# Optimization experiments

Measured on AMD Instinct MI355X. Metric: run time of the kernel, lower is better.

## Reference

```python
import jax, jax.numpy as jnp
import numpy as np

B, F, N = 16, 64, 32768
C0, C1, C2 = 64, 16, 1
TOP_K = 64
EPS = 1e-5


def setup_inputs() -> dict:
    key = jax.random.key(0)
    ks = jax.random.split(key, 6)
    def rn(k, shape, scale=1.0):
        return jax.random.normal(k, shape, dtype=jnp.float32) * scale
    return {
        "sortvec": rn(ks[0], (B, 1, F, N)),
        "input": rn(ks[1], (B, F, N)),
        # conv0: kernel (F,1), in=1, out=64 -> weight reduces to [C0, F]
        "w0": rn(ks[2], (C0, F), np.sqrt(2.0 / F)), "b0": jnp.zeros((C0,), jnp.float32),
        "w1": rn(ks[3], (C1, C0), np.sqrt(2.0 / C0)), "b1": jnp.zeros((C1,), jnp.float32),
        "w2": rn(ks[4], (C2, C1), np.sqrt(2.0 / C1)), "b2": jnp.zeros((C2,), jnp.float32),
        "g0": jnp.ones((C0,), jnp.float32), "bt0": jnp.zeros((C0,), jnp.float32),
        "g1": jnp.ones((C1,), jnp.float32), "bt1": jnp.zeros((C1,), jnp.float32),
        "g2": jnp.ones((C2,), jnp.float32), "bt2": jnp.zeros((C2,), jnp.float32),
    }


def _bn_relu(x, g, b):
    # training-mode BatchNorm2d over (B, N) per channel; x: [B, C, N]
    mu = jnp.mean(x, axis=(0, 2), keepdims=True)
    var = jnp.var(x, axis=(0, 2), keepdims=True)
    return jax.nn.relu((x - mu) * jax.lax.rsqrt(var + EPS) * g[None, :, None] + b[None, :, None])


def reference(sortvec, input, w0, b0, w1, b1, w2, b2, g0, bt0, g1, bt1, g2, bt2):
    # conv0 with kernel (F,1) collapses the feature axis: [B,1,F,N] -> [B,C0,N]
    x = jnp.einsum('bfn,of->bon', sortvec[:, 0], w0) + b0[None, :, None]
    x = _bn_relu(x, g0, bt0)
    x = _bn_relu(jnp.einsum('bcn,oc->bon', x, w1) + b1[None, :, None], g1, bt1)
    score = _bn_relu(jnp.einsum('bcn,oc->bon', x, w2) + b2[None, :, None], g2, bt2)  # [B,1,N]
    _, idx = jax.lax.top_k(score[:, 0], TOP_K)                                        # [B,K]
    sorted_input = jnp.take_along_axis(input, idx[:, None, :], axis=2)                # [B,F,K]
    sorted_score = jnp.take_along_axis(score, idx[:, None, :], axis=2)                # [B,1,K]
    feat = jnp.concatenate([sorted_input, sorted_score], axis=1)                      # [B,F+1,K]
    return feat, idx
```

## Files before the change

kernel.cpp:

```cpp
#include <hip/hip_runtime.h>


constexpr int   B_   = 16;
constexpr int   F_   = 64;
constexpr int   N_   = 32768;
constexpr int   C0_  = 64;
constexpr int   C1_  = 16;
constexpr int   K_   = 64;
constexpr long long S_ = (long long)B_ * N_;
constexpr float EPS_ = 1e-5f;

constexpr int NB0 = 1024;
constexpr int NB1 = 2048;
constexpr int NB2 = 2048;
constexpr int T64 = 8192;

__global__ __launch_bounds__(256) void k_prep(const float* __restrict__ w0,
                                              const float* __restrict__ w1,
                                              float* __restrict__ w0T,
                                              float* __restrict__ w1T) {
  int t = threadIdx.x;
  for (int e = t; e < 64 * 64; e += 256) {
    int o = e >> 6, f = e & 63;
    w0T[f * 64 + o] = w0[e];
  }
  for (int e = t; e < 16 * 64; e += 256) {
    int o = e >> 6, c = e & 63;
    w1T[c * 16 + o] = w1[e];
  }
}

__global__ __launch_bounds__(256) void k_stat0(const float* __restrict__ sv,
                                               const float* __restrict__ w0T,
                                               const float* __restrict__ b0,
                                               float* __restrict__ p0) {
  __shared__ float svt[64][64];
  const int t  = threadIdx.x;
  const int p  = t & 63;
  const int cg = __builtin_amdgcn_readfirstlane(t >> 6);

  float bb[16];
#pragma unroll
  for (int j = 0; j < 16; ++j) bb[j] = b0[cg * 16 + j];

  float s1[16], s2[16];
#pragma unroll
  for (int j = 0; j < 16; ++j) { s1[j] = 0.f; s2[j] = 0.f; }

  for (int tile = blockIdx.x; tile < T64; tile += NB0) {
    const int b  = tile >> 9;
    const int n0 = (tile & 511) << 6;
    const float* src = sv + ((long long)b * 64) * N_ + n0;
    __syncthreads();
#pragma unroll
    for (int q = 0; q < 4; ++q) {
      int e = t + q * 256;
      int f = e >> 4, c4 = (e & 15) << 2;
      *(float4*)&svt[f][c4] = *(const float4*)(src + (long long)f * N_ + c4);
    }
    __syncthreads();

    float y[16];
#pragma unroll
    for (int j = 0; j < 16; ++j) y[j] = bb[j];
    for (int f = 0; f < 64; ++f) {
      float s = svt[f][p];
      const float* wr = w0T + f * 64 + cg * 16;
#pragma unroll
      for (int j = 0; j < 16; ++j) y[j] = fmaf(wr[j], s, y[j]);
    }
#pragma unroll
    for (int j = 0; j < 16; ++j) {
      s1[j] += y[j];
      s2[j] = fmaf(y[j], y[j], s2[j]);
    }
  }

#pragma unroll
  for (int j = 0; j < 16; ++j) {
#pragma unroll
    for (int off = 32; off; off >>= 1) {
      s1[j] += __shfl_down(s1[j], off, 64);
      s2[j] += __shfl_down(s2[j], off, 64);
    }
  }
  if (p == 0) {
    float* dst = p0 + (long long)blockIdx.x * 128;
#pragma unroll
    for (int j = 0; j < 16; ++j) {
      dst[cg * 16 + j]      = s1[j];
      dst[64 + cg * 16 + j] = s2[j];
    }
  }
}

__global__ __launch_bounds__(128) void k_reduce0(const float* __restrict__ p0,
                                                 const float* __restrict__ g,
                                                 const float* __restrict__ bt,
                                                 float* __restrict__ st) {
  __shared__ float l[128];
  int j = threadIdx.x;
  float a0 = 0.f, a1 = 0.f, a2 = 0.f, a3 = 0.f;
  for (int i = 0; i < NB0; i += 4) {
    a0 += p0[(long long)(i + 0) * 128 + j];
    a1 += p0[(long long)(i + 1) * 128 + j];
    a2 += p0[(long long)(i + 2) * 128 + j];
    a3 += p0[(long long)(i + 3) * 128 + j];
  }
  l[j] = (a0 + a1) + (a2 + a3);
  __syncthreads();
  if (j < 64) {
    const float inv = 1.f / (float)S_;
    float mean = l[j] * inv;
    float ex2  = l[64 + j] * inv;
    float var  = ex2 - mean * mean;
    float sc   = g[j] * rsqrtf(var + EPS_);
    st[j]      = sc;
    st[64 + j] = bt[j] - mean * sc;
  }
}

__global__ __launch_bounds__(256) void k_layer01(const float* __restrict__ sv,
                                                 const float* __restrict__ w0T,
                                                 const float* __restrict__ b0,
                                                 const float* __restrict__ st0,
                                                 const float* __restrict__ w1T,
                                                 const float* __restrict__ b1,
                                                 float* __restrict__ y1,
                                                 float* __restrict__ p1) {
  __shared__ float svt[64][64];
  __shared__ float h0[64][64];
  const int t  = threadIdx.x;
  const int p  = t & 63;
  const int cg = __builtin_amdgcn_readfirstlane(t >> 6);

  float bb[16], sc[16], sh[16];
#pragma unroll
  for (int j = 0; j < 16; ++j) {
    bb[j] = b0[cg * 16 + j];
    sc[j] = st0[cg * 16 + j];
    sh[j] = st0[64 + cg * 16 + j];
  }
  float bb1[4];
#pragma unroll
  for (int j = 0; j < 4; ++j) bb1[j] = b1[cg * 4 + j];

  float s1[4], s2[4];
#pragma unroll
  for (int j = 0; j < 4; ++j) { s1[j] = 0.f; s2[j] = 0.f; }

  for (int tile = blockIdx.x; tile < T64; tile += NB1) {
    const int b  = tile >> 9;
    const int n0 = (tile & 511) << 6;
    const float* src = sv + ((long long)b * 64) * N_ + n0;
    __syncthreads();
#pragma unroll
    for (int q = 0; q < 4; ++q) {
      int e = t + q * 256;
      int f = e >> 4, c4 = (e & 15) << 2;
      *(float4*)&svt[f][c4] = *(const float4*)(src + (long long)f * N_ + c4);
    }
    __syncthreads();

    float y[16];
#pragma unroll
    for (int j = 0; j < 16; ++j) y[j] = bb[j];
    for (int f = 0; f < 64; ++f) {
      float s = svt[f][p];
      const float* wr = w0T + f * 64 + cg * 16;
#pragma unroll
      for (int j = 0; j < 16; ++j) y[j] = fmaf(wr[j], s, y[j]);
    }
#pragma unroll
    for (int j = 0; j < 16; ++j) {
      float h = fmaf(y[j], sc[j], sh[j]);
      h0[cg * 16 + j][p] = h > 0.f ? h : 0.f;
    }
    __syncthreads();

    float z[4];
#pragma unroll
    for (int j = 0; j < 4; ++j) z[j] = bb1[j];
    for (int f = 0; f < 64; ++f) {
      float h = h0[f][p];
      const float* wr = w1T + f * 16 + cg * 4;
#pragma unroll
      for (int j = 0; j < 4; ++j) z[j] = fmaf(wr[j], h, z[j]);
    }
#pragma unroll
    for (int j = 0; j < 4; ++j) {
      s1[j] += z[j];
      s2[j] = fmaf(z[j], z[j], s2[j]);
      y1[((long long)b * 16 + cg * 4 + j) * N_ + n0 + p] = z[j];
    }
  }

#pragma unroll
  for (int j = 0; j < 4; ++j) {
#pragma unroll
    for (int off = 32; off; off >>= 1) {
      s1[j] += __shfl_down(s1[j], off, 64);
      s2[j] += __shfl_down(s2[j], off, 64);
    }
  }
  if (p == 0) {
    float* dst = p1 + (long long)blockIdx.x * 32;
#pragma unroll
    for (int j = 0; j < 4; ++j) {
      dst[cg * 4 + j]      = s1[j];
      dst[16 + cg * 4 + j] = s2[j];
    }
  }
}

__global__ __launch_bounds__(64) void k_reduce1(const float* __restrict__ p1,
                                                const float* __restrict__ g,
                                                const float* __restrict__ bt,
                                                float* __restrict__ st) {
  __shared__ float l[32];
  int j = threadIdx.x;
  if (j < 32) {
    float a0 = 0.f, a1 = 0.f, a2 = 0.f, a3 = 0.f;
    for (int i = 0; i < NB1; i += 4) {
      a0 += p1[(long long)(i + 0) * 32 + j];
      a1 += p1[(long long)(i + 1) * 32 + j];
      a2 += p1[(long long)(i + 2) * 32 + j];
      a3 += p1[(long long)(i + 3) * 32 + j];
    }
    l[j] = (a0 + a1) + (a2 + a3);
  }
  __syncthreads();
  if (j < 16) {
    const float inv = 1.f / (float)S_;
    float mean = l[j] * inv;
    float ex2  = l[16 + j] * inv;
    float var  = ex2 - mean * mean;
    float sc   = g[j] * rsqrtf(var + EPS_);
    st[j]      = sc;
    st[16 + j] = bt[j] - mean * sc;
  }
}

__global__ __launch_bounds__(256) void k_layer2(const float* __restrict__ y1,
                                                const float* __restrict__ st1,
                                                const float* __restrict__ w2,
                                                const float* __restrict__ b2,
                                                float* __restrict__ y2,
                                                float* __restrict__ p2) {
  __shared__ float yt[16][256];
  __shared__ float ls[4], lq[4];
  const int t    = threadIdx.x;
  const int tile = blockIdx.x;
  const int b    = tile >> 7;
  const int n0   = (tile & 127) << 8;
  const float* src = y1 + ((long long)b * 16) * N_ + n0;
#pragma unroll
  for (int q = 0; q < 4; ++q) {
    int e = t + q * 256;
    int c = e >> 6, c4 = (e & 63) << 2;
    *(float4*)&yt[c][c4] = *(const float4*)(src + (long long)c * N_ + c4);
  }
  __syncthreads();

  float acc = b2[0];
#pragma unroll
  for (int c = 0; c < 16; ++c) {
    float h = fmaf(yt[c][t], st1[c], st1[16 + c]);
    h = h > 0.f ? h : 0.f;
    acc = fmaf(w2[c], h, acc);
  }
  y2[(long long)b * N_ + n0 + t] = acc;

  float ss = acc, sq = acc * acc;
#pragma unroll
  for (int off = 32; off; off >>= 1) {
    ss += __shfl_down(ss, off, 64);
    sq += __shfl_down(sq, off, 64);
  }
  int wid = t >> 6, lid = t & 63;
  if (lid == 0) { ls[wid] = ss; lq[wid] = sq; }
  __syncthreads();
  if (t == 0) {
    p2[(long long)blockIdx.x * 2 + 0] = (ls[0] + ls[1]) + (ls[2] + ls[3]);
    p2[(long long)blockIdx.x * 2 + 1] = (lq[0] + lq[1]) + (lq[2] + lq[3]);
  }
}

__global__ __launch_bounds__(1024) void k_topk(const float* __restrict__ y2,
                                               const float* __restrict__ p2,
                                               const float* __restrict__ g2,
                                               const float* __restrict__ bt2,
                                               const float* __restrict__ inp,
                                               float* __restrict__ out) {
  __shared__ float rr[1024];
  __shared__ unsigned long long wbest[16];
  __shared__ int   idxs[K_];
  __shared__ float scores[K_];
  __shared__ float s2s[2];

  const int t = threadIdx.x;
  const int b = blockIdx.x;

  {
    int comp = t >> 9;
    int j    = t & 511;
    float a = p2[(long long)(j)        * 2 + comp] +
              p2[(long long)(j + 512)  * 2 + comp] +
              p2[(long long)(j + 1024) * 2 + comp] +
              p2[(long long)(j + 1536) * 2 + comp];
    rr[t] = a;
    __syncthreads();
    for (int s = 256; s > 0; s >>= 1) {
      if (j < s) rr[t] = rr[t] + rr[t + s];
      __syncthreads();
    }
    if (t == 0) {
      const float inv = 1.f / (float)S_;
      float mean = rr[0] * inv;
      float ex2  = rr[512] * inv;
      float var  = ex2 - mean * mean;
      float scv  = g2[0] * rsqrtf(var + EPS_);
      s2s[0] = scv;
      s2s[1] = bt2[0] - mean * scv;
    }
    __syncthreads();
  }
  const float scale2 = s2s[0], shift2 = s2s[1];

  const float* yrow = y2 + (long long)b * N_;
  unsigned long long key[32];
  unsigned long long cur = 0ull;
#pragma unroll
  for (int i = 0; i < 32; ++i) {
    int idx = (i << 10) | t;
    float v = yrow[idx];
    unsigned u = __float_as_uint(v);
    u = (u & 0x80000000u) ? ~u : (u | 0x80000000u);
    unsigned long long k = ((unsigned long long)u << 32) | (unsigned)(N_ - 1 - idx);
    key[i] = k;
    cur = k > cur ? k : cur;
  }

  const int wid = t >> 6, lid = t & 63;
  for (int r = 0; r < K_; ++r) {
    unsigned long long m = cur;
#pragma unroll
    for (int off = 32; off; off >>= 1) {
      unsigned long long o = __shfl_xor(m, off, 64);
      m = o > m ? o : m;
    }
    if (lid == 0) wbest[wid] = m;
    __syncthreads();
    unsigned long long w = wbest[0];
#pragma unroll
    for (int i = 1; i < 16; ++i) {
      unsigned long long x = wbest[i];
      w = x > w ? x : w;
    }
    const int idx = N_ - 1 - (int)(w & 0xffffffffu);
    if (t == 0) {
      idxs[r] = idx;
      unsigned u = (unsigned)(w >> 32);
      u = (u & 0x80000000u) ? (u & 0x7fffffffu) : ~u;
      float v = __uint_as_float(u);
      float s = fmaf(v, scale2, shift2);
      scores[r] = s > 0.f ? s : 0.f;
    }
    if ((idx & 1023) == t) {
      const int slot = idx >> 10;
#pragma unroll
      for (int i2 = 0; i2 < 32; ++i2)
        if (i2 == slot) key[i2] = 0ull;
      unsigned long long c2 = 0ull;
#pragma unroll
      for (int i2 = 0; i2 < 32; ++i2) c2 = key[i2] > c2 ? key[i2] : c2;
      cur = c2;
    }
    __syncthreads();
  }

  const float* ib = inp + ((long long)b * 64) * N_;
  for (int e = t; e < 65 * 64; e += 1024) {
    int f = e >> 6, k = e & 63;
    float val = (f < 64) ? ib[(long long)f * N_ + idxs[k]] : scores[k];
    out[((long long)b * 65 + f) * 64 + k] = val;
  }
  if (t < K_) out[(long long)B_ * 65 * 64 + b * 64 + t] = (float)idxs[t];
}

extern "C" void kernel_launch(void* const* d_in, const int* in_sizes, int n_in,
                              void* d_out, int out_size, void* d_ws, size_t ws_size,
                              hipStream_t stream) {
  const float* sv  = (const float*)d_in[0];
  const float* inp = (const float*)d_in[1];
  const float* w0  = (const float*)d_in[2];
  const float* b0  = (const float*)d_in[3];
  const float* w1  = (const float*)d_in[4];
  const float* b1  = (const float*)d_in[5];
  const float* w2  = (const float*)d_in[6];
  const float* b2  = (const float*)d_in[7];
  const float* g0  = (const float*)d_in[8];
  const float* bt0 = (const float*)d_in[9];
  const float* g1  = (const float*)d_in[10];
  const float* bt1 = (const float*)d_in[11];
  const float* g2  = (const float*)d_in[12];
  const float* bt2 = (const float*)d_in[13];
  float* out = (float*)d_out;

  float* ws  = (float*)d_ws;
  float* y1  = ws;
  float* y2  = y1 + (size_t)S_ * 16;
  float* p0  = y2 + (size_t)S_;
  float* p1  = p0 + (size_t)NB0 * 128;
  float* p2  = p1 + (size_t)NB1 * 32;
  float* st0 = p2 + (size_t)NB2 * 2;
  float* st1 = st0 + 128;
  float* w0T = st1 + 32;
  float* w1T = w0T + 4096;

  k_prep   <<<1,    256, 0, stream>>>(w0, w1, w0T, w1T);
  k_stat0  <<<NB0,  256, 0, stream>>>(sv, w0T, b0, p0);
  k_reduce0<<<1,    128, 0, stream>>>(p0, g0, bt0, st0);
  k_layer01<<<NB1,  256, 0, stream>>>(sv, w0T, b0, st0, w1T, b1, y1, p1);
  k_reduce1<<<1,     64, 0, stream>>>(p1, g1, bt1, st1);
  k_layer2 <<<NB2,  256, 0, stream>>>(y1, st1, w2, b2, y2, p2);
  k_topk   <<<B_,  1024, 0, stream>>>(y2, p2, g2, bt2, inp, out);
}
```

Baseline: 332.2 us.

## Replace iterative block top-k with histogram threshold, candidate compaction and wave-level select

The score kernel now also builds a per-batch 4096-bin histogram of order-preserving score keys in shared memory and merges it into a global histogram. A threshold kernel then finds the bin that holds the 64th-largest score. A compaction kernel appends only the scores at or above that bin to a small per-batch candidate buffer, and a single wave selects the top 64 from those candidates. This replaces 64 block-wide argmax rounds over 32768 elements, each with barriers and only 16 blocks running. The trade-off is three extra launches, a memset, global atomics, and a fixed candidate capacity of 1024 that would silently drop entries if the threshold bin is too crowded.

```diff
diff --git a/kernel.cpp b/kernel.cpp
--- a/kernel.cpp
+++ b/kernel.cpp
@@ -2,18 +2,22 @@
 
 
 constexpr int   B_   = 16;
-constexpr int   F_   = 64;
 constexpr int   N_   = 32768;
-constexpr int   C0_  = 64;
-constexpr int   C1_  = 16;
 constexpr int   K_   = 64;
 constexpr long long S_ = (long long)B_ * N_;
 constexpr float EPS_ = 1e-5f;
 
-constexpr int NB0 = 1024;
-constexpr int NB1 = 2048;
-constexpr int NB2 = 2048;
-constexpr int T64 = 8192;
+constexpr int NB0   = 1024;
+constexpr int NB1   = 2048;
+constexpr int NB2   = 128;
+constexpr int T64   = 8192;
+constexpr int NBINS = 4096;
+constexpr int CAP   = 1024;
+
+__device__ __forceinline__ unsigned key_map(float f) {
+  unsigned u = __float_as_uint(f);
+  return (u & 0x80000000u) ? ~u : (u | 0x80000000u);
+}
 
 __global__ __launch_bounds__(256) void k_prep(const float* __restrict__ w0,
                                               const float* __restrict__ w1,
@@ -241,107 +245,169 @@
   }
 }
 
-__global__ __launch_bounds__(256) void k_layer2(const float* __restrict__ y1,
-                                                const float* __restrict__ st1,
-                                                const float* __restrict__ w2,
-                                                const float* __restrict__ b2,
-                                                float* __restrict__ y2,
-                                                float* __restrict__ p2) {
-  __shared__ float yt[16][256];
-  __shared__ float ls[4], lq[4];
-  const int t    = threadIdx.x;
-  const int tile = blockIdx.x;
-  const int b    = tile >> 7;
-  const int n0   = (tile & 127) << 8;
-  const float* src = y1 + ((long long)b * 16) * N_ + n0;
-#pragma unroll
-  for (int q = 0; q < 4; ++q) {
-    int e = t + q * 256;
-    int c = e >> 6, c4 = (e & 63) << 2;
-    *(float4*)&yt[c][c4] = *(const float4*)(src + (long long)c * N_ + c4);
-  }
+__global__ __launch_bounds__(1024) void k_layer2(const float* __restrict__ y1,
+                                                 const float* __restrict__ st1,
+                                                 const float* __restrict__ w2,
+                                                 const float* __restrict__ b2,
+                                                 float* __restrict__ y2,
+                                                 float* __restrict__ p2,
+                                                 int* __restrict__ ghist) {
+  __shared__ int hist[NBINS];
+  __shared__ float ls[16], lq[16];
+  const int t   = threadIdx.x;
+  const int blk = blockIdx.x;
+  const int b   = blk >> 3;
+  const int n0  = ((blk & 7) << 12) | (t << 2);
+
+#pragma unroll
+  for (int i = 0; i < NBINS / 1024; ++i) hist[t + i * 1024] = 0;
+
+  float sc[16], sh[16], w[16];
+#pragma unroll
+  for (int c = 0; c < 16; ++c) { sc[c] = st1[c]; sh[c] = st1[16 + c]; w[c] = w2[c]; }
+  const float bias = b2[0];
+
+  float a0 = bias, a1 = bias, a2 = bias, a3 = bias;
+  const float* base = y1 + ((long long)b * 16) * N_ + n0;
+#pragma unroll
+  for (int c = 0; c < 16; ++c) {
+    float4 v = *(const float4*)(base + (long long)c * N_);
+    float h;
+    h = fmaf(v.x, sc[c], sh[c]); h = h > 0.f ? h : 0.f; a0 = fmaf(w[c], h, a0);
+    h = fmaf(v.y, sc[c], sh[c]); h = h > 0.f ? h : 0.f; a1 = fmaf(w[c], h, a1);
+    h = fmaf(v.z, sc[c], sh[c]); h = h > 0.f ? h : 0.f; a2 = fmaf(w[c], h, a2);
+    h = fmaf(v.w, sc[c], sh[c]); h = h > 0.f ? h : 0.f; a3 = fmaf(w[c], h, a3);
+  }
+  float4 o; o.x = a0; o.y = a1; o.z = a2; o.w = a3;
+  *(float4*)(y2 + (long long)b * N_ + n0) = o;
+
   __syncthreads();
 
-  float acc = b2[0];
-#pragma unroll
-  for (int c = 0; c < 16; ++c) {
-    float h = fmaf(yt[c][t], st1[c], st1[16 + c]);
-    h = h > 0.f ? h : 0.f;
-    acc = fmaf(w2[c], h, acc);
-  }
-  y2[(long long)b * N_ + n0 + t] = acc;
-
-  float ss = acc, sq = acc * acc;
+  atomicAdd(&hist[key_map(a0) >> 20], 1);
+  atomicAdd(&hist[key_map(a1) >> 20], 1);
+  atomicAdd(&hist[key_map(a2) >> 20], 1);
+  atomicAdd(&hist[key_map(a3) >> 20], 1);
+
+  float ss = (a0 + a1) + (a2 + a3);
+  float sq = fmaf(a0, a0, fmaf(a1, a1, fmaf(a2, a2, a3 * a3)));
 #pragma unroll
   for (int off = 32; off; off >>= 1) {
     ss += __shfl_down(ss, off, 64);
     sq += __shfl_down(sq, off, 64);
   }
-  int wid = t >> 6, lid = t & 63;
+  const int wid = t >> 6, lid = t & 63;
   if (lid == 0) { ls[wid] = ss; lq[wid] = sq; }
   __syncthreads();
   if (t == 0) {
-    p2[(long long)blockIdx.x * 2 + 0] = (ls[0] + ls[1]) + (ls[2] + ls[3]);
-    p2[(long long)blockIdx.x * 2 + 1] = (lq[0] + lq[1]) + (lq[2] + lq[3]);
-  }
-}
-
-__global__ __launch_bounds__(1024) void k_topk(const float* __restrict__ y2,
-                                               const float* __restrict__ p2,
-                                               const float* __restrict__ g2,
-                                               const float* __restrict__ bt2,
-                                               const float* __restrict__ inp,
-                                               float* __restrict__ out) {
-  __shared__ float rr[1024];
-  __shared__ unsigned long long wbest[16];
-  __shared__ int   idxs[K_];
-  __shared__ float scores[K_];
-  __shared__ float s2s[2];
-
-  const int t = threadIdx.x;
-  const int b = blockIdx.x;
-
-  {
-    int comp = t >> 9;
-    int j    = t & 511;
-    float a = p2[(long long)(j)        * 2 + comp] +
-              p2[(long long)(j + 512)  * 2 + comp] +
-              p2[(long long)(j + 1024) * 2 + comp] +
-              p2[(long long)(j + 1536) * 2 + comp];
-    rr[t] = a;
-    __syncthreads();
-    for (int s = 256; s > 0; s >>= 1) {
-      if (j < s) rr[t] = rr[t] + rr[t + s];
-      __syncthreads();
-    }
-    if (t == 0) {
-      const float inv = 1.f / (float)S_;
-      float mean = rr[0] * inv;
-      float ex2  = rr[512] * inv;
-      float var  = ex2 - mean * mean;
-      float scv  = g2[0] * rsqrtf(var + EPS_);
-      s2s[0] = scv;
-      s2s[1] = bt2[0] - mean * scv;
-    }
-    __syncthreads();
-  }
-  const float scale2 = s2s[0], shift2 = s2s[1];
-
-  const float* yrow = y2 + (long long)b * N_;
-  unsigned long long key[32];
+    float Sv = 0.f, Qv = 0.f;
+#pragma unroll
+    for (int i = 0; i < 16; ++i) { Sv += ls[i]; Qv += lq[i]; }
+    p2[blk * 2 + 0] = Sv;
+    p2[blk * 2 + 1] = Qv;
+  }
+#pragma unroll
+  for (int i = 0; i < NBINS / 1024; ++i) {
+    int v = hist[t + i * 1024];
+    if (v) atomicAdd(&ghist[b * NBINS + t + i * 1024], v);
+  }
+}
+
+__global__ __launch_bounds__(256) void k_thresh(const int* __restrict__ ghist,
+                                                int* __restrict__ Tb) {
+  __shared__ int hl[NBINS + NBINS / 64];
+  const int t = threadIdx.x, b = blockIdx.x;
+  const int* h = ghist + b * NBINS;
+  for (int i = t; i < NBINS; i += 256) hl[i + (i >> 6)] = h[i];
+  __syncthreads();
+  if (t < 64) {
+    const int l = t;
+    int s = 0;
+    for (int j = 0; j < 64; ++j) s += hl[(l * 64 + j) + l];
+    int Sv = s;
+#pragma unroll
+    for (int off = 1; off < 64; off <<= 1) {
+      int v = __shfl_down(Sv, off, 64);
+      if (l + off < 64) Sv += v;
+    }
+    unsigned long long m = __ballot(Sv >= K_);
+    const int lstar = 63 - __builtin_clzll(m);
+    const int tailS = (lstar < 63) ? __shfl(Sv, lstar + 1, 64) : 0;
+    int Tj = hl[(lstar * 64 + l) + lstar];
+#pragma unroll
+    for (int off = 1; off < 64; off <<= 1) {
+      int v = __shfl_down(Tj, off, 64);
+      if (l + off < 64) Tj += v;
+    }
+    const int cge = Tj + tailS;
+    unsigned long long m2 = __ballot(cge >= K_);
+    const int jstar = 63 - __builtin_clzll(m2);
+    if (l == 0) Tb[b] = lstar * 64 + jstar;
+  }
+}
+
+__global__ __launch_bounds__(1024) void k_compact(const float* __restrict__ y2,
+                                                  const int* __restrict__ Tb,
+                                                  int* __restrict__ cnt,
+                                                  unsigned long long* __restrict__ cand) {
+  const int t = threadIdx.x, blk = blockIdx.x;
+  const int b  = blk >> 3;
+  const int n0 = ((blk & 7) << 12) | (t << 2);
+  const int T  = Tb[b];
+  float4 v = *(const float4*)(y2 + (long long)b * N_ + n0);
+  unsigned long long* cb = cand + (long long)b * CAP;
+#define DO_CAND(comp, off)                                                    \
+  {                                                                           \
+    unsigned u = key_map(comp);                                               \
+    if ((int)(u >> 20) >= T) {                                                \
+      int slot = atomicAdd(&cnt[b], 1);                                       \
+      if (slot < CAP)                                                         \
+        cb[slot] = ((unsigned long long)u << 32) |                            \
+                   (unsigned)(N_ - 1 - (n0 + off));                           \
+    }                                                                         \
+  }
+  DO_CAND(v.x, 0) DO_CAND(v.y, 1) DO_CAND(v.z, 2) DO_CAND(v.w, 3)
+#undef DO_CAND
+}
+
+__global__ __launch_bounds__(64) void k_final(const unsigned long long* __restrict__ cand,
+                                              const int* __restrict__ cnt,
+                                              const float* __restrict__ p2,
+                                              const float* __restrict__ g2,
+                                              const float* __restrict__ bt2,
+                                              const float* __restrict__ inp,
+                                              float* __restrict__ out) {
+  const int b = blockIdx.x, l = threadIdx.x;
+
+  float s1 = p2[2 * l] + p2[2 * (l + 64)];
+  float q1 = p2[2 * l + 1] + p2[2 * (l + 64) + 1];
+#pragma unroll
+  for (int off = 32; off; off >>= 1) {
+    s1 += __shfl_down(s1, off, 64);
+    q1 += __shfl_down(q1, off, 64);
+  }
+  s1 = __shfl(s1, 0, 64);
+  q1 = __shfl(q1, 0, 64);
+  const float inv = 1.f / (float)S_;
+  const float mean = s1 * inv;
+  const float var  = q1 * inv - mean * mean;
+  const float scale2 = g2[0] * rsqrtf(var + EPS_);
+  const float shift2 = bt2[0] - mean * scale2;
+
+  int cn = cnt[b];
+  if (cn > CAP) cn = CAP;
+  const unsigned long long* cb = cand + (long long)b * CAP;
+  unsigned long long k[16];
+#pragma unroll
+  for (int r = 0; r < 16; ++r) {
+    int i = l + r * 64;
+    k[r] = (i < cn) ? cb[i] : 0ull;
+  }
   unsigned long long cur = 0ull;
 #pragma unroll
-  for (int i = 0; i < 32; ++i) {
-    int idx = (i << 10) | t;
-    float v = yrow[idx];
-    unsigned u = __float_as_uint(v);
-    u = (u & 0x80000000u) ? ~u : (u | 0x80000000u);
-    unsigned long long k = ((unsigned long long)u << 32) | (unsigned)(N_ - 1 - idx);
-    key[i] = k;
-    cur = k > cur ? k : cur;
-  }
-
-  const int wid = t >> 6, lid = t & 63;
+  for (int r = 0; r < 16; ++r) cur = k[r] > cur ? k[r] : cur;
+
+  int myidx = 0;
+  unsigned mymap = 0;
   for (int r = 0; r < K_; ++r) {
     unsigned long long m = cur;
 #pragma unroll
@@ -349,43 +415,33 @@
       unsigned long long o = __shfl_xor(m, off, 64);
       m = o > m ? o : m;
     }
-    if (lid == 0) wbest[wid] = m;
-    __syncthreads();
-    unsigned long long w = wbest[0];
-#pragma unroll
-    for (int i = 1; i < 16; ++i) {
-      unsigned long long x = wbest[i];
-      w = x > w ? x : w;
-    }
-    const int idx = N_ - 1 - (int)(w & 0xffffffffu);
-    if (t == 0) {
-      idxs[r] = idx;
-      unsigned u = (unsigned)(w >> 32);
-      u = (u & 0x80000000u) ? (u & 0x7fffffffu) : ~u;
-      float v = __uint_as_float(u);
-      float s = fmaf(v, scale2, shift2);
-      scores[r] = s > 0.f ? s : 0.f;
-    }
-    if ((idx & 1023) == t) {
-      const int slot = idx >> 10;
-#pragma unroll
-      for (int i2 = 0; i2 < 32; ++i2)
-        if (i2 == slot) key[i2] = 0ull;
+    if (r == l) {
+      myidx = N_ - 1 - (int)(m & 0xffffffffu);
+      mymap = (unsigned)(m >> 32);
+    }
+    if (cur == m) {
+#pragma unroll
+      for (int r2 = 0; r2 < 16; ++r2)
+        if (k[r2] == m) k[r2] = 0ull;
       unsigned long long c2 = 0ull;
 #pragma unroll
-      for (int i2 = 0; i2 < 32; ++i2) c2 = key[i2] > c2 ? key[i2] : c2;
+      for (int r2 = 0; r2 < 16; ++r2) c2 = k[r2] > c2 ? k[r2] : c2;
       cur = c2;
     }
-    __syncthreads();
-  }
+  }
+
+  unsigned u = mymap;
+  u = (u & 0x80000000u) ? (u & 0x7fffffffu) : ~u;
+  float v = __uint_as_float(u);
+  float scv = fmaf(v, scale2, shift2);
+  scv = scv > 0.f ? scv : 0.f;
 
   const float* ib = inp + ((long long)b * 64) * N_;
-  for (int e = t; e < 65 * 64; e += 1024) {
-    int f = e >> 6, k = e & 63;
-    float val = (f < 64) ? ib[(long long)f * N_ + idxs[k]] : scores[k];
-    out[((long long)b * 65 + f) * 64 + k] = val;
-  }
-  if (t < K_) out[(long long)B_ * 65 * 64 + b * 64 + t] = (float)idxs[t];
+#pragma unroll 4
+  for (int f = 0; f < 64; ++f)
+    out[((long long)b * 65 + f) * 64 + l] = ib[(long long)f * N_ + myidx];
+  out[((long long)b * 65 + 64) * 64 + l] = scv;
+  out[(long long)B_ * 65 * 64 + b * 64 + l] = (float)myidx;
 }
 
 extern "C" void kernel_launch(void* const* d_in, const int* in_sizes, int n_in,
@@ -413,16 +469,25 @@
   float* p0  = y2 + (size_t)S_;
   float* p1  = p0 + (size_t)NB0 * 128;
   float* p2  = p1 + (size_t)NB1 * 32;
-  float* st0 = p2 + (size_t)NB2 * 2;
+  float* st0 = p2 + 256;
   float* st1 = st0 + 128;
   float* w0T = st1 + 32;
   float* w1T = w0T + 4096;
+  int*   ghist = (int*)(w1T + 1024);
+  int*   cnt   = ghist + (size_t)B_ * NBINS;
+  int*   Tb    = cnt + 16;
+  unsigned long long* cand =
+      (unsigned long long*)(Tb + 16);
+
+  hipMemsetAsync(ghist, 0, ((size_t)B_ * NBINS + 16) * sizeof(int), stream);
 
   k_prep   <<<1,    256, 0, stream>>>(w0, w1, w0T, w1T);
   k_stat0  <<<NB0,  256, 0, stream>>>(sv, w0T, b0, p0);
   k_reduce0<<<1,    128, 0, stream>>>(p0, g0, bt0, st0);
   k_layer01<<<NB1,  256, 0, stream>>>(sv, w0T, b0, st0, w1T, b1, y1, p1);
   k_reduce1<<<1,     64, 0, stream>>>(p1, g1, bt1, st1);
-  k_layer2 <<<NB2,  256, 0, stream>>>(y1, st1, w2, b2, y2, p2);
-  k_topk   <<<B_,  1024, 0, stream>>>(y2, p2, g2, bt2, inp, out);
-}
+  k_layer2 <<<NB2, 1024, 0, stream>>>(y1, st1, w2, b2, y2, p2, ghist);
+  k_thresh <<<B_,   256, 0, stream>>>(ghist, Tb);
+  k_compact<<<NB2, 1024, 0, stream>>>(y2, Tb, cnt, cand);
+  k_final  <<<B_,    64, 0, stream>>>(cand, cnt, p2, g2, bt2, inp, out);
+}
```

After: 279.6 us. -15.8%, faster.
